# Kernel tuning notes

Hardware: AMD Instinct MI355X
Metric: run time of the kernel (lower is better)

The kernel has to match this reference:

```python
import jax, jax.numpy as jnp
import numpy as np

B, L, D, H, NB = 64, 30, 512, 8, 6
AS, MT = 18, 4096
T = 3 * L
HD = D // H
EPS = 1e-3  # keras LayerNormalization default epsilon
CONV_FEAT = 7 * 7 * 64  # 84 ->(8,s4) 20 ->(4,s2) 9 ->(3,s1) 7


def setup_inputs() -> dict:
    key = jax.random.key(0)
    ks = iter(jax.random.split(key, 64))
    r = lambda *s: jax.random.normal(next(ks), s, jnp.float32) * 0.02
    inp = {
        'rtgs': jax.random.normal(next(ks), (B, L, 1), jnp.float32),
        'states': jax.random.uniform(next(ks), (B, L, 84, 84, 4), jnp.float32) * 255.0,
        'actions': jax.random.randint(next(ks), (B, L, 1), 0, AS),
        'timesteps': jax.random.randint(next(ks), (B, 1, 1), 0, MT + 1),
        # rtg embedding
        'W_rtg': r(1, D), 'b_rtg': r(D),
        # state conv stem (HWIO)
        'conv1_w': r(8, 8, 4, 32), 'conv1_b': r(32),
        'conv2_w': r(4, 4, 32, 64), 'conv2_b': r(64),
        'conv3_w': r(3, 3, 64, 64), 'conv3_b': r(64),
        'dense_s_w': r(CONV_FEAT, D), 'dense_s_b': r(D),
        # action embedding table
        'emb_a': r(AS, D),
        # positional embeddings
        'abs_pos': r(1, MT + 1, D), 'rel_pos': r(1, T + 1, D),
        # decoder blocks (stacked over NB)
        'ln1_g': 1.0 + r(NB, D), 'ln1_b': r(NB, D),
        'Wk': r(NB, D, D), 'bk': r(NB, D),
        'Wq': r(NB, D, D), 'bq': r(NB, D),
        'Wv': r(NB, D, D), 'bv': r(NB, D),
        'ln2_g': 1.0 + r(NB, D), 'ln2_b': r(NB, D),
        'W1': r(NB, D, 4 * D), 'b1': r(NB, 4 * D),
        'W2': r(NB, 4 * D, D), 'b2': r(NB, D),
        # final norm + head (no bias)
        'lnf_g': 1.0 + r(D), 'lnf_b': r(D),
        'W_head': r(D, AS),
    }
    return inp


def _conv(x, w, b, stride):
    y = jax.lax.conv_general_dilated(x, w, (stride, stride), 'VALID',
                                     dimension_numbers=('NHWC', 'HWIO', 'NHWC'))
    return jax.nn.relu(y + b)


def _layernorm(x, g, b):
    m = x.mean(-1, keepdims=True)
    v = ((x - m) ** 2).mean(-1, keepdims=True)
    return (x - m) / jnp.sqrt(v + EPS) * g + b


def _attn(x, Wk, bk, Wq, bq, Wv, bv):
    Bx, Tx, C = x.shape
    split = lambda z: z.reshape(Bx, Tx, H, HD).transpose(0, 2, 1, 3)  # (B,H,T,hd)
    k, q, v = split(x @ Wk + bk), split(x @ Wq + bq), split(x @ Wv + bv)
    # NOTE: faithful to source: scores = K @ Q^T (not Q @ K^T)
    s = jnp.einsum('bhid,bhjd->bhij', k, q) / jnp.sqrt(jnp.float32(HD))
    mask = jnp.tril(jnp.ones((Tx, Tx), bool))
    s = jnp.where(mask, s, -jnp.inf)
    w = jax.nn.softmax(s, axis=-1)
    o = jnp.einsum('bhij,bhjd->bhid', w, v)
    return o.transpose(0, 2, 1, 3).reshape(Bx, Tx, C)


def reference(rtgs, states, actions, timesteps, W_rtg, b_rtg,
              conv1_w, conv1_b, conv2_w, conv2_b, conv3_w, conv3_b,
              dense_s_w, dense_s_b, emb_a, abs_pos, rel_pos,
              ln1_g, ln1_b, Wk, bk, Wq, bq, Wv, bv,
              ln2_g, ln2_b, W1, b1, W2, b2, lnf_g, lnf_b, W_head):
    # embeddings
    rtg_e = jnp.tanh(rtgs @ W_rtg + b_rtg)                       # (B,L,D)
    s = states.reshape(B * L, 84, 84, 4) / 255.0
    s = _conv(s, conv1_w, conv1_b, 4)
    s = _conv(s, conv2_w, conv2_b, 2)
    s = _conv(s, conv3_w, conv3_b, 1)
    st_e = jnp.tanh(s.reshape(B, L, -1) @ dense_s_w + dense_s_b)  # (B,L,D)
    a_e = jnp.tanh(emb_a[actions[..., 0]])                        # (B,L,D)
    # positional: abs gathered at start timestep + relative
    abs_e = abs_pos[0][timesteps[:, 0, 0]][:, None, :]            # (B,1,D)
    pos = rel_pos[:, :T, :] + abs_e                               # (B,3L,D)
    # interleave (rtg, state, action) per timestep
    tokens = jnp.stack([rtg_e, st_e, a_e], axis=2).reshape(B, T, D)
    x = tokens + pos
    for i in range(NB):
        h = _layernorm(x, ln1_g[i], ln1_b[i])
        x = x + _attn(h, Wk[i], bk[i], Wq[i], bq[i], Wv[i], bv[i])
        h = _layernorm(x, ln2_g[i], ln2_b[i])
        x = x + jax.nn.gelu(h @ W1[i] + b1[i], approximate=False) @ W2[i] + b2[i]
    x = _layernorm(x, lnf_g, lnf_b)
    logits = x @ W_head                                           # (B,3L,AS)
    return logits[:, 1::3, :]                                     # state positions -> (B,L,AS)
```

## Files before the change

### kernel.cpp

```cpp
#include <hip/hip_runtime.h>
#include <hip/hip_bf16.h>

typedef __attribute__((ext_vector_type(8))) __bf16 bf16x8;
typedef __attribute__((ext_vector_type(4))) float f32x4;

#define ACT_NONE 0
#define ACT_RELU 1
#define ACT_GELU 2
#define ACT_TANH 3
#define OUT_F32 0
#define OUT_BF16 1
#define OUT_ADD 2

__device__ __forceinline__ void gll16(const void* g, void* l) {
  __builtin_amdgcn_global_load_lds(
      reinterpret_cast<const __attribute__((address_space(1))) unsigned int*>(
          reinterpret_cast<unsigned long long>(g)),
      reinterpret_cast<__attribute__((address_space(3))) unsigned int*>(
          reinterpret_cast<unsigned long long>(l)),
      16, 0, 0);
}

template<int MODE, int K>
__device__ __forceinline__ size_t a_rowbase(int m) {
  if constexpr (MODE == 0) {
    return (size_t)m * K;
  } else if constexpr (MODE == 1) {
    int img = m / 400; int p = m - img * 400; int oy = p / 20; int ox = p - oy * 20;
    return (size_t)img * 28224 + oy * 1344 + ox * 16;
  } else if constexpr (MODE == 2) {
    int img = m / 81; int p = m - img * 81; int oy = p / 9; int ox = p - oy * 9;
    return (size_t)img * 12800 + oy * 1280 + ox * 64;
  } else {
    int img = m / 49; int p = m - img * 49; int oy = p / 7; int ox = p - oy * 7;
    return (size_t)img * 5184 + oy * 576 + ox * 64;
  }
}
template<int MODE>
__device__ __forceinline__ int f_koff(int kb) {
  if constexpr (MODE == 0) return kb;
  else if constexpr (MODE == 2) return (kb >> 7) * 640 + ((kb >> 5) & 3) * 32;
  else return kb + (kb / 192) * 384;
}

__device__ __forceinline__ bf16x8 ld8f(const float* f) {
  float4 a = *(const float4*)f;
  float4 b = *(const float4*)(f + 4);
  bf16x8 r;
  r[0] = (__bf16)a.x; r[1] = (__bf16)a.y; r[2] = (__bf16)a.z; r[3] = (__bf16)a.w;
  r[4] = (__bf16)b.x; r[5] = (__bf16)b.y; r[6] = (__bf16)b.z; r[7] = (__bf16)b.w;
  return r;
}

__device__ __forceinline__ float act_apply(float v, int ACT) {
  if (ACT == ACT_RELU) return fmaxf(v, 0.f);
  if (ACT == ACT_GELU) return 0.5f * v * (1.f + erff(v * 0.70710678118f));
  if (ACT == ACT_TANH) return tanhf(v);
  return v;
}

template<int MODE, int TM, int TN, int WM, int WN, int K, int ACT, int OUTM, int LDC>
__global__ __launch_bounds__(256) void gemm_k(const __bf16* __restrict__ A,
                                              const __bf16* __restrict__ BT,
                                              const float* __restrict__ bias,
                                              void* __restrict__ C) {
  constexpr int SM = TM / WM, SN = TN / WN;
  constexpr int AM = SM / 16, AN = SN / 16;
  constexpr int TA = TM / 64, TB = TN / 64;
  __shared__ __align__(16) __bf16 As[TM * 32];
  __shared__ __align__(16) __bf16 Bs[TN * 32];
  const int tid = threadIdx.x;
  const int wave = tid >> 6, lane = tid & 63;
  const int quad = lane >> 4, l16 = lane & 15;
  const int wr = wave % WM, wc = wave / WM;
  const int m0 = blockIdx.x * TM, n0 = blockIdx.y * TN;
  const int lrow = lane >> 2, lkc = lane & 3;

  const __bf16* ga[TA];
  const __bf16* gb[TB];
#pragma unroll
  for (int t = 0; t < TA; ++t)
    ga[t] = A + a_rowbase<MODE, K>(m0 + (wave + 4 * t) * 16 + lrow) + lkc * 8;
#pragma unroll
  for (int t = 0; t < TB; ++t)
    gb[t] = BT + (size_t)(n0 + (wave + 4 * t) * 16 + lrow) * K + lkc * 8;

  f32x4 acc[AM][AN] = {};
  for (int kt = 0; kt < K / 32; ++kt) {
    const int kb = kt * 32;
    const int fa = f_koff<MODE>(kb);
    __syncthreads();
#pragma unroll
    for (int t = 0; t < TA; ++t)
      gll16(ga[t] + fa, &As[(wave + 4 * t) * 16 * 32]);
#pragma unroll
    for (int t = 0; t < TB; ++t)
      gll16(gb[t] + kb, &Bs[(wave + 4 * t) * 16 * 32]);
    __syncthreads();
    bf16x8 af[AM], bf[AN];
#pragma unroll
    for (int mt = 0; mt < AM; ++mt)
      af[mt] = *(const bf16x8*)&As[(wr * SM + mt * 16 + l16) * 32 + quad * 8];
#pragma unroll
    for (int nt = 0; nt < AN; ++nt)
      bf[nt] = *(const bf16x8*)&Bs[(wc * SN + nt * 16 + l16) * 32 + quad * 8];
#pragma unroll
    for (int mt = 0; mt < AM; ++mt)
#pragma unroll
      for (int nt = 0; nt < AN; ++nt)
        acc[mt][nt] = __builtin_amdgcn_mfma_f32_16x16x32_bf16(af[mt], bf[nt], acc[mt][nt], 0, 0, 0);
  }

#pragma unroll
  for (int nt = 0; nt < AN; ++nt) {
    const int col = n0 + wc * SN + nt * 16 + l16;
    const float bvl = bias[col];
#pragma unroll
    for (int mt = 0; mt < AM; ++mt) {
#pragma unroll
      for (int r = 0; r < 4; ++r) {
        const int row = m0 + wr * SM + mt * 16 + quad * 4 + r;
        float v = act_apply(acc[mt][nt][r] + bvl, ACT);
        const size_t off = (size_t)row * LDC + col;
        if constexpr (OUTM == OUT_F32) ((float*)C)[off] = v;
        else if constexpr (OUTM == OUT_BF16) ((__bf16*)C)[off] = (__bf16)v;
        else ((float*)C)[off] += v;
      }
    }
  }
}

__global__ __launch_bounds__(256) void conv1_k(const float* __restrict__ A,
                                               const __bf16* __restrict__ BT,
                                               const float* __restrict__ bias,
                                               __bf16* __restrict__ C) {
  __shared__ __align__(16) __bf16 As[128 * 32];
  __shared__ __align__(16) __bf16 Bs[32 * 32];
  const int tid = threadIdx.x;
  const int wave = tid >> 6, lane = tid & 63;
  const int quad = lane >> 4, l16 = lane & 15;
  const int m0 = blockIdx.x * 128;
  const int lrow = lane >> 2, lkc = lane & 3;
  const int r0 = tid >> 2, k0o = (tid & 3) * 8;
  const int r1 = r0 + 64;
  const size_t ar0 = a_rowbase<1, 256>(m0 + r0);
  const size_t ar1 = a_rowbase<1, 256>(m0 + r1);
  const __bf16* gB = BT + (size_t)(wave * 16 + lrow) * 256 + lkc * 8;

  f32x4 acc[2][2] = {};
  bf16x8 a0 = ld8f(A + ar0 + k0o);
  bf16x8 a1 = ld8f(A + ar1 + k0o);
  for (int kt = 0; kt < 8; ++kt) {
    const int kb = kt * 32;
    __syncthreads();
    if (wave < 2) gll16(gB + kb, &Bs[wave * 16 * 32]);
    *(bf16x8*)&As[r0 * 32 + k0o] = a0;
    *(bf16x8*)&As[r1 * 32 + k0o] = a1;
    __syncthreads();
    if (kt < 7) {
      const int fa = (kt + 1) * 336;
      a0 = ld8f(A + ar0 + fa + k0o);
      a1 = ld8f(A + ar1 + fa + k0o);
    }
    bf16x8 af[2], bf[2];
#pragma unroll
    for (int mt = 0; mt < 2; ++mt)
      af[mt] = *(const bf16x8*)&As[(wave * 32 + mt * 16 + l16) * 32 + quad * 8];
#pragma unroll
    for (int nt = 0; nt < 2; ++nt)
      bf[nt] = *(const bf16x8*)&Bs[(nt * 16 + l16) * 32 + quad * 8];
#pragma unroll
    for (int mt = 0; mt < 2; ++mt)
#pragma unroll
      for (int nt = 0; nt < 2; ++nt)
        acc[mt][nt] = __builtin_amdgcn_mfma_f32_16x16x32_bf16(af[mt], bf[nt], acc[mt][nt], 0, 0, 0);
  }
#pragma unroll
  for (int nt = 0; nt < 2; ++nt) {
    const int col = nt * 16 + l16;
    const float bvl = bias[col];
#pragma unroll
    for (int mt = 0; mt < 2; ++mt) {
#pragma unroll
      for (int r = 0; r < 4; ++r) {
        const int row = m0 + wave * 32 + mt * 16 + quad * 4 + r;
        C[(size_t)row * 32 + col] = (__bf16)fmaxf(acc[mt][nt][r] + bvl, 0.f);
      }
    }
  }
}

template<typename TO>
__global__ void transpose_pad(const float* __restrict__ src, TO* __restrict__ dst,
                              int R, int C, int Cpad, long long sz, long long dz, float scale) {
  src += blockIdx.z * sz; dst += blockIdx.z * dz;
  __shared__ float t[32][33];
  const int tx = threadIdx.x, ty = threadIdx.y;
  const int r0 = blockIdx.x * 32, c0 = blockIdx.y * 32;
  for (int i = ty; i < 32; i += 8) {
    int r = r0 + i, c = c0 + tx;
    t[i][tx] = (r < R && c < C) ? src[(size_t)r * C + c] : 0.f;
  }
  __syncthreads();
  for (int i = ty; i < 32; i += 8) {
    int c = c0 + i, r = r0 + tx;
    if (c < Cpad && r < R)
      dst[(size_t)c * R + r] = (c < C) ? (TO)(t[tx][i] * scale) : (TO)0.f;
  }
}

__global__ void biascat_k(const float* bk, const float* bq, const float* bv, float* dst) {
  const int i = blockIdx.x;
  for (int d = threadIdx.x; d < 512; d += 256) {
    dst[i * 1536 + d] = bk[i * 512 + d];
    dst[i * 1536 + 512 + d] = bq[i * 512 + d];
    dst[i * 1536 + 1024 + d] = bv[i * 512 + d];
  }
}

__global__ void embed_k(const float* __restrict__ rtgs, const int* __restrict__ actions,
                        const int* __restrict__ timesteps, const float* __restrict__ W_rtg,
                        const float* __restrict__ b_rtg, const float* __restrict__ emb_a,
                        const float* __restrict__ abs_pos, const float* __restrict__ rel_pos,
                        const float* __restrict__ ste, float* __restrict__ x) {
  const int idx = blockIdx.x * 256 + threadIdx.x;
  const int d = idx & 511; const int rb = idx >> 9;
  const int b = rb / 90, t = rb - b * 90;
  const int l = t / 3, r = t - l * 3;
  const float pos = rel_pos[t * 512 + d] + abs_pos[(size_t)timesteps[b] * 512 + d];
  float tok;
  if (r == 0) tok = tanhf(rtgs[b * 30 + l] * W_rtg[d] + b_rtg[d]);
  else if (r == 1) tok = ste[(size_t)(b * 30 + l) * 512 + d];
  else tok = tanhf(emb_a[actions[b * 30 + l] * 512 + d]);
  x[idx] = tok + pos;
}

__global__ __launch_bounds__(256) void ln_k(const float* __restrict__ x, const float* __restrict__ g,
                                            const float* __restrict__ bb, __bf16* __restrict__ h) {
  const int row = blockIdx.x * 4 + (threadIdx.x >> 6);
  const int lane = threadIdx.x & 63;
  const float* xr = x + (size_t)row * 512;
  float4 a = *(const float4*)&xr[lane * 8];
  float4 c = *(const float4*)&xr[lane * 8 + 4];
  float vv[8] = {a.x, a.y, a.z, a.w, c.x, c.y, c.z, c.w};
  float s = 0.f, q = 0.f;
#pragma unroll
  for (int j = 0; j < 8; ++j) { s += vv[j]; q += vv[j] * vv[j]; }
  for (int o = 32; o; o >>= 1) { s += __shfl_xor(s, o); q += __shfl_xor(q, o); }
  const float mean = s * (1.f / 512.f);
  const float var = q * (1.f / 512.f) - mean * mean;
  const float rstd = rsqrtf(var + 1e-3f);
  float4 g1 = *(const float4*)&g[lane * 8];
  float4 g2 = *(const float4*)&g[lane * 8 + 4];
  float4 b1 = *(const float4*)&bb[lane * 8];
  float4 b2 = *(const float4*)&bb[lane * 8 + 4];
  float gg[8] = {g1.x, g1.y, g1.z, g1.w, g2.x, g2.y, g2.z, g2.w};
  float bbv[8] = {b1.x, b1.y, b1.z, b1.w, b2.x, b2.y, b2.z, b2.w};
  bf16x8 ov;
#pragma unroll
  for (int j = 0; j < 8; ++j)
    ov[j] = (__bf16)((vv[j] - mean) * rstd * gg[j] + bbv[j]);
  *(bf16x8*)&h[(size_t)row * 512 + lane * 8] = ov;
}

__global__ __launch_bounds__(256) void attn_k(const __bf16* __restrict__ qkv, float* __restrict__ x) {
  __shared__ __align__(16) char smem[64512];
  __bf16* kS = (__bf16*)smem;
  __bf16* qS = (__bf16*)(smem + 13824);
  __bf16* wS = (__bf16*)smem;
  float* sS = (float*)(smem + 27648);
  __bf16* vT = (__bf16*)(smem + 27648);

  const int tid = threadIdx.x;
  const int b = blockIdx.x >> 3, h = blockIdx.x & 7;
  const int wave = tid >> 6, lane = tid & 63, quad = lane >> 4, l16 = lane & 15;
  const size_t rowbase = (size_t)b * 90 * 1536 + h * 64;

  for (int c = tid; c < 768; c += 256) {
    const int t = c >> 3, d8 = (c & 7) * 8;
    bf16x8 kv, qv;
#pragma unroll
    for (int j = 0; j < 8; ++j) { kv[j] = (__bf16)0.f; qv[j] = (__bf16)0.f; }
    if (t < 90) {
      const __bf16* src = qkv + rowbase + (size_t)t * 1536 + d8;
      kv = *(const bf16x8*)src;
      qv = *(const bf16x8*)(src + 512);
    }
    *(bf16x8*)&kS[t * 72 + d8] = kv;
    *(bf16x8*)&qS[t * 72 + d8] = qv;
  }
  __syncthreads();

  for (int tt = wave; tt < 36; tt += 4) {
    const int it = tt / 6, jt = tt - it * 6;
    f32x4 acc = {0.f, 0.f, 0.f, 0.f};
#pragma unroll
    for (int ks = 0; ks < 2; ++ks) {
      bf16x8 af = *(const bf16x8*)&kS[(it * 16 + l16) * 72 + ks * 32 + quad * 8];
      bf16x8 bq = *(const bf16x8*)&qS[(jt * 16 + l16) * 72 + ks * 32 + quad * 8];
      acc = __builtin_amdgcn_mfma_f32_16x16x32_bf16(af, bq, acc, 0, 0, 0);
    }
    const int col = jt * 16 + l16;
#pragma unroll
    for (int r = 0; r < 4; ++r) {
      const int row = it * 16 + quad * 4 + r;
      sS[row * 96 + col] = (col <= row && col < 90) ? acc[r] * 0.125f : -1e30f;
    }
  }
  __syncthreads();

  for (int row = wave; row < 96; row += 4) {
    const float e0 = sS[row * 96 + lane];
    const float e1 = (lane < 32) ? sS[row * 96 + 64 + lane] : -1e30f;
    float m = fmaxf(e0, e1);
    for (int o = 32; o; o >>= 1) m = fmaxf(m, __shfl_xor(m, o));
    const float p0 = __expf(e0 - m);
    const float p1 = (lane < 32) ? __expf(e1 - m) : 0.f;
    float s = p0 + p1;
    for (int o = 32; o; o >>= 1) s += __shfl_xor(s, o);
    const float inv = 1.f / s;
    wS[row * 104 + lane] = (__bf16)(p0 * inv);
    if (lane < 32) wS[row * 104 + 64 + lane] = (__bf16)(p1 * inv);
  }
  __syncthreads();

  for (int c = tid; c < 768; c += 256) {
    const int t = c >> 3, d8 = (c & 7) * 8;
    bf16x8 vv;
#pragma unroll
    for (int j = 0; j < 8; ++j) vv[j] = (__bf16)0.f;
    if (t < 90) vv = *(const bf16x8*)(qkv + rowbase + (size_t)t * 1536 + 1024 + d8);
#pragma unroll
    for (int j = 0; j < 8; ++j) vT[(d8 + j) * 104 + t] = vv[j];
  }
  __syncthreads();

  for (int tt = wave; tt < 24; tt += 4) {
    const int it = tt >> 2, dt = tt & 3;
    f32x4 acc = {0.f, 0.f, 0.f, 0.f};
#pragma unroll
    for (int ks = 0; ks < 3; ++ks) {
      bf16x8 aw = *(const bf16x8*)&wS[(it * 16 + l16) * 104 + ks * 32 + quad * 8];
      bf16x8 bv = *(const bf16x8*)&vT[(dt * 16 + l16) * 104 + ks * 32 + quad * 8];
      acc = __builtin_amdgcn_mfma_f32_16x16x32_bf16(aw, bv, acc, 0, 0, 0);
    }
    const int d = dt * 16 + l16;
#pragma unroll
    for (int r = 0; r < 4; ++r) {
      const int i = it * 16 + quad * 4 + r;
      if (i < 90) {
        float* p = x + (size_t)(b * 90 + i) * 512 + h * 64 + d;
        *p += acc[r];
      }
    }
  }
}

__global__ __launch_bounds__(64) void head_k(const float* __restrict__ x, const float* __restrict__ g,
                                             const float* __restrict__ bb, const float* __restrict__ whT,
                                             float* __restrict__ out) {
  const int m = blockIdx.x;
  const int b = m / 30, l = m - b * 30;
  const float* xr = x + (size_t)(b * 90 + 3 * l + 1) * 512;
  const int lane = threadIdx.x;
  float4 a = *(const float4*)&xr[lane * 8];
  float4 c = *(const float4*)&xr[lane * 8 + 4];
  float vv[8] = {a.x, a.y, a.z, a.w, c.x, c.y, c.z, c.w};
  float s = 0.f, q = 0.f;
#pragma unroll
  for (int j = 0; j < 8; ++j) { s += vv[j]; q += vv[j] * vv[j]; }
  for (int o = 32; o; o >>= 1) { s += __shfl_xor(s, o); q += __shfl_xor(q, o); }
  const float mean = s * (1.f / 512.f);
  const float var = q * (1.f / 512.f) - mean * mean;
  const float rstd = rsqrtf(var + 1e-3f);
  float4 g1 = *(const float4*)&g[lane * 8];
  float4 g2 = *(const float4*)&g[lane * 8 + 4];
  float4 b1 = *(const float4*)&bb[lane * 8];
  float4 b2 = *(const float4*)&bb[lane * 8 + 4];
  float gg[8] = {g1.x, g1.y, g1.z, g1.w, g2.x, g2.y, g2.z, g2.w};
  float bbv[8] = {b1.x, b1.y, b1.z, b1.w, b2.x, b2.y, b2.z, b2.w};
#pragma unroll
  for (int j = 0; j < 8; ++j)
    vv[j] = (vv[j] - mean) * rstd * gg[j] + bbv[j];
  for (int aa = 0; aa < 18; ++aa) {
    float4 w1v = *(const float4*)&whT[aa * 512 + lane * 8];
    float4 w2v = *(const float4*)&whT[aa * 512 + lane * 8 + 4];
    float ww[8] = {w1v.x, w1v.y, w1v.z, w1v.w, w2v.x, w2v.y, w2v.z, w2v.w};
    float d = 0.f;
#pragma unroll
    for (int j = 0; j < 8; ++j) d += vv[j] * ww[j];
    for (int o = 32; o; o >>= 1) d += __shfl_xor(d, o);
    if (lane == 0) out[m * 18 + aa] = d;
  }
}

extern "C" void kernel_launch(void* const* d_in, const int* in_sizes, int n_in,
                              void* d_out, int out_size, void* d_ws, size_t ws_size,
                              hipStream_t stream) {
  const float* rtgs = (const float*)d_in[0];
  const float* states = (const float*)d_in[1];
  const int* actions = (const int*)d_in[2];
  const int* timesteps = (const int*)d_in[3];
  const float* W_rtg = (const float*)d_in[4];
  const float* b_rtg = (const float*)d_in[5];
  const float* conv1_w = (const float*)d_in[6];
  const float* conv1_b = (const float*)d_in[7];
  const float* conv2_w = (const float*)d_in[8];
  const float* conv2_b = (const float*)d_in[9];
  const float* conv3_w = (const float*)d_in[10];
  const float* conv3_b = (const float*)d_in[11];
  const float* dense_s_w = (const float*)d_in[12];
  const float* dense_s_b = (const float*)d_in[13];
  const float* emb_a = (const float*)d_in[14];
  const float* abs_pos = (const float*)d_in[15];
  const float* rel_pos = (const float*)d_in[16];
  const float* ln1_g = (const float*)d_in[17];
  const float* ln1_b = (const float*)d_in[18];
  const float* Wk = (const float*)d_in[19];
  const float* bk = (const float*)d_in[20];
  const float* Wq = (const float*)d_in[21];
  const float* bq = (const float*)d_in[22];
  const float* Wv = (const float*)d_in[23];
  const float* bv = (const float*)d_in[24];
  const float* ln2_g = (const float*)d_in[25];
  const float* ln2_b = (const float*)d_in[26];
  const float* W1 = (const float*)d_in[27];
  const float* b1 = (const float*)d_in[28];
  const float* W2 = (const float*)d_in[29];
  const float* b2 = (const float*)d_in[30];
  const float* lnf_g = (const float*)d_in[31];
  const float* lnf_b = (const float*)d_in[32];
  const float* W_head = (const float*)d_in[33];
  float* out = (float*)d_out;

  char* W = (char*)d_ws;
  float* x = (float*)(W + 0);
  __bf16* h = (__bf16*)(W + 11796480);
  __bf16* qkvT = (__bf16*)(W + 17694720);
  __bf16* w1T = (__bf16*)(W + 27131904);
  __bf16* w2T = (__bf16*)(W + 39714816);
  __bf16* dswT = (__bf16*)(W + 52297728);
  __bf16* c1wT = (__bf16*)(W + 55508992);
  __bf16* c2wT = (__bf16*)(W + 55574528);
  __bf16* c3wT = (__bf16*)(W + 55705600);
  float* whT = (float*)(W + 55853056);
  float* bqkv = (float*)(W + 55889920);
  __bf16* c1out = (__bf16*)(W + 55926784);
  __bf16* c2out = (__bf16*)(W + 105078784);
  __bf16* c3out = (__bf16*)(W + 55926784);
  float* ste = (float*)(W + 67969024);
  __bf16* qkvb = (__bf16*)(W + 55926784);
  __bf16* mlph = (__bf16*)(W + 73621504);

  const dim3 tb(32, 8);
  transpose_pad<__bf16><<<dim3(8, 4, 1), tb, 0, stream>>>(conv1_w, c1wT, 256, 32, 128, 0, 0, 1.f / 255.f);
  transpose_pad<__bf16><<<dim3(16, 4, 1), tb, 0, stream>>>(conv2_w, c2wT, 512, 64, 128, 0, 0, 1.f);
  transpose_pad<__bf16><<<dim3(18, 4, 1), tb, 0, stream>>>(conv3_w, c3wT, 576, 64, 128, 0, 0, 1.f);
  transpose_pad<__bf16><<<dim3(98, 16, 1), tb, 0, stream>>>(dense_s_w, dswT, 3136, 512, 512, 0, 0, 1.f);
  transpose_pad<__bf16><<<dim3(16, 16, 6), tb, 0, stream>>>(Wk, qkvT, 512, 512, 512, 512 * 512, 1536 * 512, 1.f);
  transpose_pad<__bf16><<<dim3(16, 16, 6), tb, 0, stream>>>(Wq, qkvT + 512 * 512, 512, 512, 512, 512 * 512, 1536 * 512, 1.f);
  transpose_pad<__bf16><<<dim3(16, 16, 6), tb, 0, stream>>>(Wv, qkvT + 1024 * 512, 512, 512, 512, 512 * 512, 1536 * 512, 1.f);
  transpose_pad<__bf16><<<dim3(16, 64, 6), tb, 0, stream>>>(W1, w1T, 512, 2048, 2048, 512 * 2048, 2048 * 512, 1.f);
  transpose_pad<__bf16><<<dim3(64, 16, 6), tb, 0, stream>>>(W2, w2T, 2048, 512, 512, 2048 * 512, 512 * 2048, 1.f);
  transpose_pad<float><<<dim3(16, 1, 1), tb, 0, stream>>>(W_head, whT, 512, 18, 18, 0, 0, 1.f);
  biascat_k<<<6, 256, 0, stream>>>(bk, bq, bv, bqkv);

  conv1_k<<<6000, 256, 0, stream>>>(states, c1wT, conv1_b, c1out);
  gemm_k<2, 128, 64, 2, 2, 512, ACT_RELU, OUT_BF16, 64><<<dim3(1215, 1), 256, 0, stream>>>(c1out, c2wT, conv2_b, c2out);
  gemm_k<3, 128, 64, 2, 2, 576, ACT_RELU, OUT_BF16, 64><<<dim3(735, 1), 256, 0, stream>>>(c2out, c3wT, conv3_b, c3out);
  gemm_k<0, 64, 64, 2, 2, 3136, ACT_TANH, OUT_F32, 512><<<dim3(30, 8), 256, 0, stream>>>(c3out, dswT, dense_s_b, (void*)ste);

  embed_k<<<11520, 256, 0, stream>>>(rtgs, actions, timesteps, W_rtg, b_rtg, emb_a, abs_pos, rel_pos, ste, x);

  for (int i = 0; i < 6; ++i) {
    ln_k<<<1440, 256, 0, stream>>>(x, ln1_g + i * 512, ln1_b + i * 512, h);
    gemm_k<0, 128, 128, 2, 2, 512, ACT_NONE, OUT_BF16, 1536><<<dim3(45, 12), 256, 0, stream>>>(
        h, qkvT + (size_t)i * 1536 * 512, bqkv + i * 1536, qkvb);
    attn_k<<<512, 256, 0, stream>>>(qkvb, x);
    ln_k<<<1440, 256, 0, stream>>>(x, ln2_g + i * 512, ln2_b + i * 512, h);
    gemm_k<0, 128, 128, 2, 2, 512, ACT_GELU, OUT_BF16, 2048><<<dim3(45, 16), 256, 0, stream>>>(
        h, w1T + (size_t)i * 2048 * 512, b1 + i * 2048, mlph);
    gemm_k<0, 64, 128, 2, 2, 2048, ACT_NONE, OUT_ADD, 512><<<dim3(90, 4), 256, 0, stream>>>(
        mlph, w2T + (size_t)i * 2048 * 512, b2 + i * 512, x);
  }

  head_k<<<1920, 64, 0, stream>>>(x, lnf_g, lnf_b, whT, out);
}
```

Before: 1.392 ms.

## Register-prefetch GEMM staging, split-K W2 with atomics, merge weight prep kernels

Replaces the direct global-to-LDS loads in the GEMM and conv1 kernels with register-staged loads that prefetch the next K tile while the current one is computed. LDS rows are padded to 40 elements to reduce bank conflicts. The second MLP GEMM is split two ways along K, with the partial sums atomically added into the residual to raise occupancy. All weight transposes and the bias concatenation are merged into one prep kernel, and the head weights are stored as bf16. The costs are atomic traffic, a non-deterministic summation order, and more register pressure.

```diff
diff --git a/kernel.cpp b/kernel.cpp
--- a/kernel.cpp
+++ b/kernel.cpp
@@ -11,15 +11,9 @@
 #define OUT_F32 0
 #define OUT_BF16 1
 #define OUT_ADD 2
-
-__device__ __forceinline__ void gll16(const void* g, void* l) {
-  __builtin_amdgcn_global_load_lds(
-      reinterpret_cast<const __attribute__((address_space(1))) unsigned int*>(
-          reinterpret_cast<unsigned long long>(g)),
-      reinterpret_cast<__attribute__((address_space(3))) unsigned int*>(
-          reinterpret_cast<unsigned long long>(l)),
-      16, 0, 0);
-}
+#define OUT_ATOMIC 3
+
+#define LDST 40
 
 template<int MODE, int K>
 __device__ __forceinline__ size_t a_rowbase(int m) {
@@ -37,10 +31,11 @@
   }
 }
 template<int MODE>
-__device__ __forceinline__ int f_koff(int kb) {
-  if constexpr (MODE == 0) return kb;
-  else if constexpr (MODE == 2) return (kb >> 7) * 640 + ((kb >> 5) & 3) * 32;
-  else return kb + (kb / 192) * 384;
+__device__ __forceinline__ int a_koff(int k) {
+  if constexpr (MODE == 0) return k;
+  else if constexpr (MODE == 1) return (k >> 5) * 336 + (k & 31);
+  else if constexpr (MODE == 2) return (k >> 7) * 640 + ((k >> 5) & 3) * 32 + (k & 31);
+  else { int ky = k / 192; int r = k - ky * 192; return ky * 576 + r; }
 }
 
 __device__ __forceinline__ bf16x8 ld8f(const float* f) {
@@ -59,51 +54,73 @@
   return v;
 }
 
-template<int MODE, int TM, int TN, int WM, int WN, int K, int ACT, int OUTM, int LDC>
-__global__ __launch_bounds__(256) void gemm_k(const __bf16* __restrict__ A,
-                                              const __bf16* __restrict__ BT,
-                                              const float* __restrict__ bias,
-                                              void* __restrict__ C) {
+template<int MODE, int TM, int TN, int WM, int WN, int K, int ACT, int OUTM, int LDC, int NSPLIT>
+__global__ __launch_bounds__(256) void gemm_rs(const __bf16* __restrict__ A,
+                                               const __bf16* __restrict__ BT,
+                                               const float* __restrict__ bias,
+                                               void* __restrict__ C) {
   constexpr int SM = TM / WM, SN = TN / WN;
   constexpr int AM = SM / 16, AN = SN / 16;
-  constexpr int TA = TM / 64, TB = TN / 64;
-  __shared__ __align__(16) __bf16 As[TM * 32];
-  __shared__ __align__(16) __bf16 Bs[TN * 32];
+  constexpr int CA = TM / 64, CB = TN / 64;
+  constexpr int KS = K / NSPLIT;
+  __shared__ __align__(16) __bf16 As[TM * LDST];
+  __shared__ __align__(16) __bf16 Bs[TN * LDST];
   const int tid = threadIdx.x;
   const int wave = tid >> 6, lane = tid & 63;
   const int quad = lane >> 4, l16 = lane & 15;
   const int wr = wave % WM, wc = wave / WM;
   const int m0 = blockIdx.x * TM, n0 = blockIdx.y * TN;
-  const int lrow = lane >> 2, lkc = lane & 3;
-
-  const __bf16* ga[TA];
-  const __bf16* gb[TB];
-#pragma unroll
-  for (int t = 0; t < TA; ++t)
-    ga[t] = A + a_rowbase<MODE, K>(m0 + (wave + 4 * t) * 16 + lrow) + lkc * 8;
-#pragma unroll
-  for (int t = 0; t < TB; ++t)
-    gb[t] = BT + (size_t)(n0 + (wave + 4 * t) * 16 + lrow) * K + lkc * 8;
+  const int ks0 = blockIdx.z * KS;
+
+  size_t abase[CA]; int akc[CA], alds[CA];
+  const __bf16* bptr[CB]; int blds[CB];
+#pragma unroll
+  for (int t = 0; t < CA; ++t) {
+    const int idx = tid + 256 * t, r = idx >> 2, kc = (idx & 3) * 8;
+    abase[t] = a_rowbase<MODE, K>(m0 + r);
+    akc[t] = kc;
+    alds[t] = r * LDST + kc;
+  }
+#pragma unroll
+  for (int t = 0; t < CB; ++t) {
+    const int idx = tid + 256 * t, r = idx >> 2, kc = (idx & 3) * 8;
+    bptr[t] = BT + (size_t)(n0 + r) * K + ks0 + kc;
+    blds[t] = r * LDST + kc;
+  }
 
   f32x4 acc[AM][AN] = {};
-  for (int kt = 0; kt < K / 32; ++kt) {
-    const int kb = kt * 32;
-    const int fa = f_koff<MODE>(kb);
+  bf16x8 av[CA], bvv[CB];
+#pragma unroll
+  for (int t = 0; t < CA; ++t)
+    av[t] = *(const bf16x8*)(A + abase[t] + a_koff<MODE>(ks0 + akc[t]));
+#pragma unroll
+  for (int t = 0; t < CB; ++t)
+    bvv[t] = *(const bf16x8*)bptr[t];
+
+  constexpr int NK = KS / 32;
+  for (int kt = 0; kt < NK; ++kt) {
     __syncthreads();
 #pragma unroll
-    for (int t = 0; t < TA; ++t)
-      gll16(ga[t] + fa, &As[(wave + 4 * t) * 16 * 32]);
-#pragma unroll
-    for (int t = 0; t < TB; ++t)
-      gll16(gb[t] + kb, &Bs[(wave + 4 * t) * 16 * 32]);
+    for (int t = 0; t < CA; ++t) *(bf16x8*)&As[alds[t]] = av[t];
+#pragma unroll
+    for (int t = 0; t < CB; ++t) *(bf16x8*)&Bs[blds[t]] = bvv[t];
     __syncthreads();
+    if (kt + 1 < NK) {
+      const int kb = (kt + 1) * 32;
+#pragma unroll
+      for (int t = 0; t < CA; ++t)
+        av[t] = *(const bf16x8*)(A + abase[t] + a_koff<MODE>(ks0 + kb + akc[t]));
+#pragma unroll
+      for (int t = 0; t < CB; ++t)
+        bvv[t] = *(const bf16x8*)(bptr[t] + kb);
+    }
     bf16x8 af[AM], bf[AN];
 #pragma unroll
     for (int mt = 0; mt < AM; ++mt)
-      af[mt] = *(const bf16x8*)&As[(wr * SM + mt * 16 + l16) * 32 + quad * 8];
+      af[mt] = *(const bf16x8*)&As[(wr * SM + mt * 16 + l16) * LDST + quad * 8];
 #pragma unroll
     for (int nt = 0; nt < AN; ++nt)
-      bf[nt] = *(const bf16x8*)&Bs[(wc * SN + nt * 16 + l16) * 32 + quad * 8];
+      bf[nt] = *(const bf16x8*)&Bs[(wc * SN + nt * 16 + l16) * LDST + quad * 8];
 #pragma unroll
     for (int mt = 0; mt < AM; ++mt)
 #pragma unroll
@@ -114,7 +131,7 @@
 #pragma unroll
   for (int nt = 0; nt < AN; ++nt) {
     const int col = n0 + wc * SN + nt * 16 + l16;
-    const float bvl = bias[col];
+    const float bvl = (NSPLIT == 1 || blockIdx.z == 0) ? bias[col] : 0.f;
 #pragma unroll
     for (int mt = 0; mt < AM; ++mt) {
 #pragma unroll
@@ -124,7 +141,8 @@
         const size_t off = (size_t)row * LDC + col;
         if constexpr (OUTM == OUT_F32) ((float*)C)[off] = v;
         else if constexpr (OUTM == OUT_BF16) ((__bf16*)C)[off] = (__bf16)v;
-        else ((float*)C)[off] += v;
+        else if constexpr (OUTM == OUT_ADD) ((float*)C)[off] += v;
+        else atomicAdd(&((float*)C)[off], v);
       }
     }
   }
@@ -134,41 +152,42 @@
                                                const __bf16* __restrict__ BT,
                                                const float* __restrict__ bias,
                                                __bf16* __restrict__ C) {
-  __shared__ __align__(16) __bf16 As[128 * 32];
-  __shared__ __align__(16) __bf16 Bs[32 * 32];
+  __shared__ __align__(16) __bf16 As[128 * LDST];
+  __shared__ __align__(16) __bf16 Bs[32 * LDST];
   const int tid = threadIdx.x;
   const int wave = tid >> 6, lane = tid & 63;
   const int quad = lane >> 4, l16 = lane & 15;
   const int m0 = blockIdx.x * 128;
-  const int lrow = lane >> 2, lkc = lane & 3;
   const int r0 = tid >> 2, k0o = (tid & 3) * 8;
   const int r1 = r0 + 64;
   const size_t ar0 = a_rowbase<1, 256>(m0 + r0);
   const size_t ar1 = a_rowbase<1, 256>(m0 + r1);
-  const __bf16* gB = BT + (size_t)(wave * 16 + lrow) * 256 + lkc * 8;
+  const __bf16* bp = BT + (size_t)r0 * 256 + k0o;
 
   f32x4 acc[2][2] = {};
   bf16x8 a0 = ld8f(A + ar0 + k0o);
   bf16x8 a1 = ld8f(A + ar1 + k0o);
+  bf16x8 b0;
+  if (tid < 128) b0 = *(const bf16x8*)bp;
   for (int kt = 0; kt < 8; ++kt) {
-    const int kb = kt * 32;
     __syncthreads();
-    if (wave < 2) gll16(gB + kb, &Bs[wave * 16 * 32]);
-    *(bf16x8*)&As[r0 * 32 + k0o] = a0;
-    *(bf16x8*)&As[r1 * 32 + k0o] = a1;
+    *(bf16x8*)&As[r0 * LDST + k0o] = a0;
+    *(bf16x8*)&As[r1 * LDST + k0o] = a1;
+    if (tid < 128) *(bf16x8*)&Bs[r0 * LDST + k0o] = b0;
     __syncthreads();
     if (kt < 7) {
       const int fa = (kt + 1) * 336;
       a0 = ld8f(A + ar0 + fa + k0o);
       a1 = ld8f(A + ar1 + fa + k0o);
+      if (tid < 128) b0 = *(const bf16x8*)(bp + (kt + 1) * 32);
     }
     bf16x8 af[2], bf[2];
 #pragma unroll
     for (int mt = 0; mt < 2; ++mt)
-      af[mt] = *(const bf16x8*)&As[(wave * 32 + mt * 16 + l16) * 32 + quad * 8];
+      af[mt] = *(const bf16x8*)&As[(wave * 32 + mt * 16 + l16) * LDST + quad * 8];
 #pragma unroll
     for (int nt = 0; nt < 2; ++nt)
-      bf[nt] = *(const bf16x8*)&Bs[(nt * 16 + l16) * 32 + quad * 8];
+      bf[nt] = *(const bf16x8*)&Bs[(nt * 16 + l16) * LDST + quad * 8];
 #pragma unroll
     for (int mt = 0; mt < 2; ++mt)
 #pragma unroll
@@ -190,13 +209,11 @@
   }
 }
 
-template<typename TO>
-__global__ void transpose_pad(const float* __restrict__ src, TO* __restrict__ dst,
-                              int R, int C, int Cpad, long long sz, long long dz, float scale) {
-  src += blockIdx.z * sz; dst += blockIdx.z * dz;
-  __shared__ float t[32][33];
-  const int tx = threadIdx.x, ty = threadIdx.y;
-  const int r0 = blockIdx.x * 32, c0 = blockIdx.y * 32;
+__device__ __forceinline__ void tp32(const float* __restrict__ src, __bf16* __restrict__ dst,
+                                     int R, int C, int bx, int by, float scale, float (*t)[33]) {
+  const int tid = threadIdx.x;
+  const int tx = tid & 31, ty = tid >> 5;
+  const int r0 = bx * 32, c0 = by * 32;
   for (int i = ty; i < 32; i += 8) {
     int r = r0 + i, c = c0 + tx;
     t[i][tx] = (r < R && c < C) ? src[(size_t)r * C + c] : 0.f;
@@ -204,17 +221,58 @@
   __syncthreads();
   for (int i = ty; i < 32; i += 8) {
     int c = c0 + i, r = r0 + tx;
-    if (c < Cpad && r < R)
-      dst[(size_t)c * R + r] = (c < C) ? (TO)(t[tx][i] * scale) : (TO)0.f;
-  }
-}
-
-__global__ void biascat_k(const float* bk, const float* bq, const float* bv, float* dst) {
-  const int i = blockIdx.x;
-  for (int d = threadIdx.x; d < 512; d += 256) {
-    dst[i * 1536 + d] = bk[i * 512 + d];
-    dst[i * 1536 + 512 + d] = bq[i * 512 + d];
-    dst[i * 1536 + 1024 + d] = bv[i * 512 + d];
+    if (c < C && r < R) dst[(size_t)c * R + r] = (__bf16)(t[tx][i] * scale);
+  }
+}
+
+__global__ void prep_k(const float* conv1_w, const float* conv2_w, const float* conv3_w,
+                       const float* dense_s_w, const float* Wk, const float* Wq, const float* Wv,
+                       const float* W1, const float* W2, const float* W_head,
+                       const float* bk, const float* bq, const float* bv,
+                       __bf16* c1wT, __bf16* c2wT, __bf16* c3wT, __bf16* dswT,
+                       __bf16* qkvT, __bf16* w1T, __bf16* w2T, __bf16* whT, float* bqkv) {
+  __shared__ float t[32][33];
+  int b = blockIdx.x;
+  if (b < 8) { tp32(conv1_w, c1wT, 256, 32, b, 0, 1.f / 255.f, t); return; }
+  b -= 8;
+  if (b < 32) { tp32(conv2_w, c2wT, 512, 64, b >> 1, b & 1, 1.f, t); return; }
+  b -= 32;
+  if (b < 36) { tp32(conv3_w, c3wT, 576, 64, b >> 1, b & 1, 1.f, t); return; }
+  b -= 36;
+  if (b < 1568) { tp32(dense_s_w, dswT, 3136, 512, b >> 4, b & 15, 1.f, t); return; }
+  b -= 1568;
+  if (b < 4608) {
+    const int g = b >> 11, rem = b & 2047;
+    const int gb = b / 1536, r2 = b - gb * 1536;
+    const float* srcs[3] = {Wk, Wq, Wv};
+    const int z = r2 >> 8, r3 = r2 & 255;
+    tp32(srcs[gb] + (size_t)z * 262144, qkvT + (size_t)z * 786432 + (size_t)gb * 262144,
+         512, 512, r3 >> 4, r3 & 15, 1.f, t);
+    (void)g; (void)rem;
+    return;
+  }
+  b -= 4608;
+  if (b < 6144) {
+    const int z = b >> 10, r3 = b & 1023;
+    tp32(W1 + (size_t)z * 1048576, w1T + (size_t)z * 1048576, 512, 2048, r3 >> 6, r3 & 63, 1.f, t);
+    return;
+  }
+  b -= 6144;
+  if (b < 6144) {
+    const int z = b >> 10, r3 = b & 1023;
+    tp32(W2 + (size_t)z * 1048576, w2T + (size_t)z * 1048576, 2048, 512, r3 >> 4, r3 & 15, 1.f, t);
+    return;
+  }
+  b -= 6144;
+  if (b < 16) { tp32(W_head, whT, 512, 18, b, 0, 1.f, t); return; }
+  b -= 16;
+  for (int idx = threadIdx.x; idx < 9216; idx += 256) {
+    const int z = idx / 1536, d = idx - z * 1536;
+    float v;
+    if (d < 512) v = bk[z * 512 + d];
+    else if (d < 1024) v = bq[z * 512 + d - 512];
+    else v = bv[z * 512 + d - 1024];
+    bqkv[idx] = v;
   }
 }
 
@@ -357,7 +415,7 @@
 }
 
 __global__ __launch_bounds__(64) void head_k(const float* __restrict__ x, const float* __restrict__ g,
-                                             const float* __restrict__ bb, const float* __restrict__ whT,
+                                             const float* __restrict__ bb, const __bf16* __restrict__ whT,
                                              float* __restrict__ out) {
   const int m = blockIdx.x;
   const int b = m / 30, l = m - b * 30;
@@ -383,12 +441,10 @@
   for (int j = 0; j < 8; ++j)
     vv[j] = (vv[j] - mean) * rstd * gg[j] + bbv[j];
   for (int aa = 0; aa < 18; ++aa) {
-    float4 w1v = *(const float4*)&whT[aa * 512 + lane * 8];
-    float4 w2v = *(const float4*)&whT[aa * 512 + lane * 8 + 4];
-    float ww[8] = {w1v.x, w1v.y, w1v.z, w1v.w, w2v.x, w2v.y, w2v.z, w2v.w};
+    bf16x8 w = *(const bf16x8*)&whT[aa * 512 + lane * 8];
     float d = 0.f;
 #pragma unroll
-    for (int j = 0; j < 8; ++j) d += vv[j] * ww[j];
+    for (int j = 0; j < 8; ++j) d += vv[j] * (float)w[j];
     for (int o = 32; o; o >>= 1) d += __shfl_xor(d, o);
     if (lane == 0) out[m * 18 + aa] = d;
   }
@@ -443,7 +499,7 @@
   __bf16* c1wT = (__bf16*)(W + 55508992);
   __bf16* c2wT = (__bf16*)(W + 55574528);
   __bf16* c3wT = (__bf16*)(W + 55705600);
-  float* whT = (float*)(W + 55853056);
+  __bf16* whT = (__bf16*)(W + 55853056);
   float* bqkv = (float*)(W + 55889920);
   __bf16* c1out = (__bf16*)(W + 55926784);
   __bf16* c2out = (__bf16*)(W + 105078784);
@@ -452,35 +508,29 @@
   __bf16* qkvb = (__bf16*)(W + 55926784);
   __bf16* mlph = (__bf16*)(W + 73621504);
 
-  const dim3 tb(32, 8);
-  transpose_pad<__bf16><<<dim3(8, 4, 1), tb, 0, stream>>>(conv1_w, c1wT, 256, 32, 128, 0, 0, 1.f / 255.f);
-  transpose_pad<__bf16><<<dim3(16, 4, 1), tb, 0, stream>>>(conv2_w, c2wT, 512, 64, 128, 0, 0, 1.f);
-  transpose_pad<__bf16><<<dim3(18, 4, 1), tb, 0, stream>>>(conv3_w, c3wT, 576, 64, 128, 0, 0, 1.f);
-  transpose_pad<__bf16><<<dim3(98, 16, 1), tb, 0, stream>>>(dense_s_w, dswT, 3136, 512, 512, 0, 0, 1.f);
-  transpose_pad<__bf16><<<dim3(16, 16, 6), tb, 0, stream>>>(Wk, qkvT, 512, 512, 512, 512 * 512, 1536 * 512, 1.f);
-  transpose_pad<__bf16><<<dim3(16, 16, 6), tb, 0, stream>>>(Wq, qkvT + 512 * 512, 512, 512, 512, 512 * 512, 1536 * 512, 1.f);
-  transpose_pad<__bf16><<<dim3(16, 16, 6), tb, 0, stream>>>(Wv, qkvT + 1024 * 512, 512, 512, 512, 512 * 512, 1536 * 512, 1.f);
-  transpose_pad<__bf16><<<dim3(16, 64, 6), tb, 0, stream>>>(W1, w1T, 512, 2048, 2048, 512 * 2048, 2048 * 512, 1.f);
-  transpose_pad<__bf16><<<dim3(64, 16, 6), tb, 0, stream>>>(W2, w2T, 2048, 512, 512, 2048 * 512, 512 * 2048, 1.f);
-  transpose_pad<float><<<dim3(16, 1, 1), tb, 0, stream>>>(W_head, whT, 512, 18, 18, 0, 0, 1.f);
-  biascat_k<<<6, 256, 0, stream>>>(bk, bq, bv, bqkv);
+  prep_k<<<18557, 256, 0, stream>>>(conv1_w, conv2_w, conv3_w, dense_s_w, Wk, Wq, Wv, W1, W2,
+                                    W_head, bk, bq, bv, c1wT, c2wT, c3wT, dswT, qkvT, w1T, w2T,
+                                    whT, bqkv);
 
   conv1_k<<<6000, 256, 0, stream>>>(states, c1wT, conv1_b, c1out);
-  gemm_k<2, 128, 64, 2, 2, 512, ACT_RELU, OUT_BF16, 64><<<dim3(1215, 1), 256, 0, stream>>>(c1out, c2wT, conv2_b, c2out);
-  gemm_k<3, 128, 64, 2, 2, 576, ACT_RELU, OUT_BF16, 64><<<dim3(735, 1), 256, 0, stream>>>(c2out, c3wT, conv3_b, c3out);
-  gemm_k<0, 64, 64, 2, 2, 3136, ACT_TANH, OUT_F32, 512><<<dim3(30, 8), 256, 0, stream>>>(c3out, dswT, dense_s_b, (void*)ste);
+  gemm_rs<2, 128, 64, 2, 2, 512, ACT_RELU, OUT_BF16, 64, 1><<<dim3(1215, 1), 256, 0, stream>>>(
+      c1out, c2wT, conv2_b, c2out);
+  gemm_rs<3, 128, 64, 2, 2, 576, ACT_RELU, OUT_BF16, 64, 1><<<dim3(735, 1), 256, 0, stream>>>(
+      c2out, c3wT, conv3_b, c3out);
+  gemm_rs<0, 64, 64, 2, 2, 3136, ACT_TANH, OUT_F32, 512, 1><<<dim3(30, 8), 256, 0, stream>>>(
+      c3out, dswT, dense_s_b, (void*)ste);
 
   embed_k<<<11520, 256, 0, stream>>>(rtgs, actions, timesteps, W_rtg, b_rtg, emb_a, abs_pos, rel_pos, ste, x);
 
   for (int i = 0; i < 6; ++i) {
     ln_k<<<1440, 256, 0, stream>>>(x, ln1_g + i * 512, ln1_b + i * 512, h);
-    gemm_k<0, 128, 128, 2, 2, 512, ACT_NONE, OUT_BF16, 1536><<<dim3(45, 12), 256, 0, stream>>>(
+    gemm_rs<0, 128, 128, 2, 2, 512, ACT_NONE, OUT_BF16, 1536, 1><<<dim3(45, 12), 256, 0, stream>>>(
         h, qkvT + (size_t)i * 1536 * 512, bqkv + i * 1536, qkvb);
     attn_k<<<512, 256, 0, stream>>>(qkvb, x);
     ln_k<<<1440, 256, 0, stream>>>(x, ln2_g + i * 512, ln2_b + i * 512, h);
-    gemm_k<0, 128, 128, 2, 2, 512, ACT_GELU, OUT_BF16, 2048><<<dim3(45, 16), 256, 0, stream>>>(
+    gemm_rs<0, 128, 128, 2, 2, 512, ACT_GELU, OUT_BF16, 2048, 1><<<dim3(45, 16), 256, 0, stream>>>(
         h, w1T + (size_t)i * 2048 * 512, b1 + i * 2048, mlph);
-    gemm_k<0, 64, 128, 2, 2, 2048, ACT_NONE, OUT_ADD, 512><<<dim3(90, 4), 256, 0, stream>>>(
+    gemm_rs<0, 64, 128, 2, 2, 2048, ACT_NONE, OUT_ATOMIC, 512, 2><<<dim3(90, 4, 2), 256, 0, stream>>>(
         mlph, w2T + (size_t)i * 2048 * 512, b2 + i * 512, x);
   }
 
```

New measurement: 1.398 ms. About the same (+0.5%).
